# Optimization experiments

Measured on AMD Instinct MI355X. Metric: run time of the kernel, lower is better.

The kernel has to match this reference:

```python
import jax, jax.numpy as jnp
import numpy as np

NUM_HEADS = 4
HEAD_DIM = 64
RHO = 0.1  # threshold_rho


def setup_inputs() -> dict:
    key = jax.random.key(0)
    k0, k1, k2, k3, k4 = jax.random.split(key, 5)
    B, L, D = 2, 225, 256  # grid_size=15 -> L=225
    Hd = NUM_HEADS * HEAD_DIM
    w_scale = 1.0 / np.sqrt(D)
    return {
        "x": jax.random.normal(k0, (B, L, D), dtype=jnp.float32),
        "Wq": jax.random.normal(k1, (Hd, D), dtype=jnp.float32) * w_scale,
        "Wk": jax.random.normal(k2, (Hd, D), dtype=jnp.float32) * w_scale,
        "Wv": jax.random.normal(k3, (Hd, D), dtype=jnp.float32) * w_scale,
        "Wo": jax.random.normal(k4, (D, Hd), dtype=jnp.float32) * w_scale,
    }


def reference(x, Wq, Wk, Wv, Wo):
    B, L, D = x.shape
    H, d = NUM_HEADS, HEAD_DIM
    # Projections (torch Linear: y = x @ W.T), split heads -> [B,H,L,d]
    q = (x @ Wq.T).reshape(B, L, H, d).transpose(0, 2, 1, 3)
    k = (x @ Wk.T).reshape(B, L, H, d).transpose(0, 2, 1, 3)
    v = (x @ Wv.T).reshape(B, L, H, d).transpose(0, 2, 1, 3)

    # Raw attention scores S = Q K^T  [B,H,L,L]
    S = jnp.einsum('bhid,bhjd->bhij', q, k)

    # Adjacency build: for each key column j, U_j = s_j s_j^T / d, zero diag,
    # keep entries > rho; A = mean over j. Vectorized over j: [B,H,Li,Lk,Lj].
    eye = jnp.eye(L, dtype=S.dtype)
    U = S[:, :, :, None, :] * S[:, :, None, :, :] / d      # [B,H,i,k,j]
    U = U * (1.0 - eye)[None, None, :, :, None]            # zero (i==k) diag
    A = jnp.where(U > RHO, U, 0.0).sum(axis=-1) / L        # [B,H,L,L]

    # Normalize: A_hat = D^-1/2 (A + I) D^-1/2
    A_tilde = A + eye
    deg = jnp.clip(A_tilde.sum(axis=-1, keepdims=True), 1e-6, None)
    d_inv_sqrt = deg ** -0.5
    A_hat = d_inv_sqrt * A_tilde * jnp.swapaxes(d_inv_sqrt, -1, -2)

    # Jump: Phi(S) = A_hat S A_hat^T, then scale and softmax-attend
    S_jump = jnp.einsum('bhij,bhjk,bhlk->bhil', A_hat, S, A_hat) / np.sqrt(d)
    attn = jax.nn.softmax(S_jump, axis=-1)
    out = jnp.einsum('bhij,bhjd->bhid', attn, v)           # [B,H,L,d]
    out = out.transpose(0, 2, 1, 3).reshape(B, L, H * d)
    return out @ Wo.T
```

## Files before the change

### kernel.cpp

```cpp
#include <hip/hip_runtime.h>
#include <math.h>

#define B_  2
#define L_  225
#define D_  256
#define H_  4
#define DH_ 64
#define BH_ (B_*H_)
#define M_  (B_*L_)
#define LL_ (L_*L_)
#define RHO 0.1f
#define INV_D 0.015625f
#define INV_L (1.0f/225.0f)
#define INV_SQRT_D 0.125f

__global__ __launch_bounds__(256) void k_qkv(
    const float* __restrict__ x, const float* __restrict__ Wq,
    const float* __restrict__ Wk, const float* __restrict__ Wv,
    float* __restrict__ q, float* __restrict__ k, float* __restrict__ v)
{
    const int which = blockIdx.z;
    const float* W = (which == 0) ? Wq : (which == 1) ? Wk : Wv;
    float* out = (which == 0) ? q : (which == 1) ? k : v;
    const int m0 = blockIdx.x * 32;
    const int n0 = blockIdx.y * 32;
    __shared__ float Xs[32][33];
    __shared__ float Ws[32][33];
    const int t = threadIdx.x;
    const int ty = t >> 4, tx = t & 15;
    float acc[2][2] = {};
    for (int kt = 0; kt < D_; kt += 32) {
        #pragma unroll
        for (int i = 0; i < 4; ++i) {
            int li = t + i * 256;
            int r = li >> 5, c = li & 31;
            int m = m0 + r;
            Xs[r][c] = (m < M_) ? x[m * D_ + kt + c] : 0.f;
            Ws[r][c] = W[(n0 + r) * D_ + kt + c];
        }
        __syncthreads();
        #pragma unroll
        for (int kk = 0; kk < 32; ++kk) {
            float a0 = Xs[ty*2+0][kk], a1 = Xs[ty*2+1][kk];
            float b0 = Ws[tx*2+0][kk], b1 = Ws[tx*2+1][kk];
            acc[0][0] += a0*b0; acc[0][1] += a0*b1;
            acc[1][0] += a1*b0; acc[1][1] += a1*b1;
        }
        __syncthreads();
    }
    #pragma unroll
    for (int i = 0; i < 2; ++i) {
        int m = m0 + ty*2 + i;
        if (m >= M_) continue;
        int b = m / L_, l = m % L_;
        #pragma unroll
        for (int j = 0; j < 2; ++j) {
            int n = n0 + tx*2 + j;
            int h = n >> 6, dd = n & 63;
            out[((b * H_ + h) * L_ + l) * DH_ + dd] = acc[i][j];
        }
    }
}

__global__ __launch_bounds__(256) void k_scores(
    const float* __restrict__ q, const float* __restrict__ kk_,
    float* __restrict__ S)
{
    const int bh = blockIdx.z;
    const int i0 = blockIdx.x * 32, j0 = blockIdx.y * 32;
    __shared__ float Qs[32][65], Ks[32][65];
    const float* qb = q + bh * L_ * DH_;
    const float* kb = kk_ + bh * L_ * DH_;
    const int t = threadIdx.x;
    #pragma unroll
    for (int i = 0; i < 8; ++i) {
        int li = t + i * 256;
        int r = li >> 6, c = li & 63;
        Qs[r][c] = (i0 + r < L_) ? qb[(i0 + r) * DH_ + c] : 0.f;
        Ks[r][c] = (j0 + r < L_) ? kb[(j0 + r) * DH_ + c] : 0.f;
    }
    __syncthreads();
    const int ty = t >> 4, tx = t & 15;
    float acc[2][2] = {};
    #pragma unroll
    for (int c = 0; c < 64; ++c) {
        float a0 = Qs[ty*2+0][c], a1 = Qs[ty*2+1][c];
        float b0 = Ks[tx*2+0][c], b1 = Ks[tx*2+1][c];
        acc[0][0] += a0*b0; acc[0][1] += a0*b1;
        acc[1][0] += a1*b0; acc[1][1] += a1*b1;
    }
    float* Sb = S + bh * LL_;
    #pragma unroll
    for (int i = 0; i < 2; ++i) {
        int gi = i0 + ty*2 + i;
        if (gi >= L_) continue;
        #pragma unroll
        for (int j = 0; j < 2; ++j) {
            int gj = j0 + tx*2 + j;
            if (gj < L_) Sb[gi * L_ + gj] = acc[i][j];
        }
    }
}

__global__ __launch_bounds__(256) void k_adj(
    const float* __restrict__ S, float* __restrict__ A)
{
    const int bh = blockIdx.z;
    const int i0 = blockIdx.x * 32, k0 = blockIdx.y * 32;
    __shared__ float Si[32][65], Sk[32][65];
    const float* Sb = S + bh * LL_;
    const int t = threadIdx.x;
    const int ii = t & 31, kk0 = (t >> 5) * 4;
    float acc[4] = {};
    for (int jc = 0; jc < L_; jc += 64) {
        #pragma unroll
        for (int i = 0; i < 8; ++i) {
            int li = t + i * 256;
            int r = li >> 6, c = li & 63;
            int j = jc + c;
            Si[r][c] = (i0 + r < L_ && j < L_) ? Sb[(i0 + r) * L_ + j] : 0.f;
            Sk[r][c] = (k0 + r < L_ && j < L_) ? Sb[(k0 + r) * L_ + j] : 0.f;
        }
        __syncthreads();
        #pragma unroll 8
        for (int j = 0; j < 64; ++j) {
            float si = Si[ii][j];
            #pragma unroll
            for (int c = 0; c < 4; ++c) {
                float u = si * Sk[kk0 + c][j] * INV_D;
                acc[c] += (u > RHO) ? u : 0.f;
            }
        }
        __syncthreads();
    }
    int gi = i0 + ii;
    if (gi < L_) {
        float* Ab = A + bh * LL_ + gi * L_;
        #pragma unroll
        for (int c = 0; c < 4; ++c) {
            int gk = k0 + kk0 + c;
            if (gk < L_) Ab[gk] = (gi == gk) ? 0.f : acc[c] * INV_L;
        }
    }
}

__global__ __launch_bounds__(256) void k_dinv(
    const float* __restrict__ A, float* __restrict__ dinv)
{
    int bh = blockIdx.x;
    int i = threadIdx.x;
    if (i >= L_) return;
    const float* Ab = A + bh * LL_ + i * L_;
    float s = 1.0f;
    for (int kx = 0; kx < L_; ++kx) s += Ab[kx];
    s = fmaxf(s, 1e-6f);
    dinv[bh * L_ + i] = 1.0f / sqrtf(s);
}

__global__ __launch_bounds__(256) void k_ahat(
    const float* __restrict__ A, const float* __restrict__ dinv,
    float* __restrict__ Ahat)
{
    int e = blockIdx.x * 256 + threadIdx.x;
    if (e >= BH_ * LL_) return;
    int bh = e / LL_;
    int rem = e - bh * LL_;
    int r = rem / L_;
    int c = rem - r * L_;
    float val = A[e] + ((r == c) ? 1.f : 0.f);
    Ahat[e] = val * dinv[bh * L_ + r] * dinv[bh * L_ + c];
}

__global__ __launch_bounds__(256) void k_m1(
    const float* __restrict__ Ahat, const float* __restrict__ S,
    float* __restrict__ M1)
{
    const int bh = blockIdx.z;
    const int i0 = blockIdx.x * 32, c0 = blockIdx.y * 32;
    __shared__ float As[32][33], Bs[32][33];
    const float* Ab = Ahat + bh * LL_;
    const float* Sb = S + bh * LL_;
    const int t = threadIdx.x;
    const int ty = t >> 4, tx = t & 15;
    float acc[2][2] = {};
    for (int jt = 0; jt < L_; jt += 32) {
        #pragma unroll
        for (int i = 0; i < 4; ++i) {
            int li = t + i * 256;
            int r = li >> 5, c = li & 31;
            As[r][c] = (i0 + r < L_ && jt + c < L_) ? Ab[(i0 + r) * L_ + jt + c] : 0.f;
            Bs[r][c] = (jt + r < L_ && c0 + c < L_) ? Sb[(jt + r) * L_ + c0 + c] : 0.f;
        }
        __syncthreads();
        #pragma unroll
        for (int kk = 0; kk < 32; ++kk) {
            float a0 = As[ty*2+0][kk], a1 = As[ty*2+1][kk];
            float b0 = Bs[kk][tx*2+0], b1 = Bs[kk][tx*2+1];
            acc[0][0] += a0*b0; acc[0][1] += a0*b1;
            acc[1][0] += a1*b0; acc[1][1] += a1*b1;
        }
        __syncthreads();
    }
    float* Mb = M1 + bh * LL_;
    #pragma unroll
    for (int i = 0; i < 2; ++i) {
        int gi = i0 + ty*2 + i;
        if (gi >= L_) continue;
        #pragma unroll
        for (int j = 0; j < 2; ++j) {
            int gc = c0 + tx*2 + j;
            if (gc < L_) Mb[gi * L_ + gc] = acc[i][j];
        }
    }
}

__global__ __launch_bounds__(256) void k_sjump(
    const float* __restrict__ M1, const float* __restrict__ Ahat,
    float* __restrict__ attn)
{
    const int bh = blockIdx.z;
    const int i0 = blockIdx.x * 32, l0 = blockIdx.y * 32;
    __shared__ float As[32][33], Bs[32][33];
    const float* Mb = M1 + bh * LL_;
    const float* Ab = Ahat + bh * LL_;
    const int t = threadIdx.x;
    const int ty = t >> 4, tx = t & 15;
    float acc[2][2] = {};
    for (int jt = 0; jt < L_; jt += 32) {
        #pragma unroll
        for (int i = 0; i < 4; ++i) {
            int li = t + i * 256;
            int r = li >> 5, c = li & 31;
            As[r][c] = (i0 + r < L_ && jt + c < L_) ? Mb[(i0 + r) * L_ + jt + c] : 0.f;
            Bs[r][c] = (l0 + r < L_ && jt + c < L_) ? Ab[(l0 + r) * L_ + jt + c] : 0.f;
        }
        __syncthreads();
        #pragma unroll
        for (int kk = 0; kk < 32; ++kk) {
            float a0 = As[ty*2+0][kk], a1 = As[ty*2+1][kk];
            float b0 = Bs[tx*2+0][kk], b1 = Bs[tx*2+1][kk];
            acc[0][0] += a0*b0; acc[0][1] += a0*b1;
            acc[1][0] += a1*b0; acc[1][1] += a1*b1;
        }
        __syncthreads();
    }
    float* ob = attn + bh * LL_;
    #pragma unroll
    for (int i = 0; i < 2; ++i) {
        int gi = i0 + ty*2 + i;
        if (gi >= L_) continue;
        #pragma unroll
        for (int j = 0; j < 2; ++j) {
            int gl = l0 + tx*2 + j;
            if (gl < L_) ob[gi * L_ + gl] = acc[i][j] * INV_SQRT_D;
        }
    }
}

__global__ __launch_bounds__(256) void k_softmax(float* __restrict__ attn)
{
    const int bh = blockIdx.y, i = blockIdx.x;
    float* row = attn + bh * LL_ + i * L_;
    const int t = threadIdx.x;
    __shared__ float red[256];
    float v = (t < L_) ? row[t] : -INFINITY;
    red[t] = v;
    __syncthreads();
    for (int s = 128; s > 0; s >>= 1) {
        if (t < s) red[t] = fmaxf(red[t], red[t + s]);
        __syncthreads();
    }
    float m = red[0];
    __syncthreads();
    float e = (t < L_) ? expf(v - m) : 0.f;
    red[t] = e;
    __syncthreads();
    for (int s = 128; s > 0; s >>= 1) {
        if (t < s) red[t] += red[t + s];
        __syncthreads();
    }
    float inv = 1.0f / red[0];
    if (t < L_) row[t] = e * inv;
}

__global__ __launch_bounds__(256) void k_av(
    const float* __restrict__ attn, const float* __restrict__ v,
    float* __restrict__ oh)
{
    const int bh = blockIdx.y, i0 = blockIdx.x * 32;
    __shared__ float As[32][33];
    __shared__ float Vs[32][64];
    const float* ab = attn + bh * LL_;
    const float* vb = v + bh * L_ * DH_;
    const int t = threadIdx.x;
    const int dd = t & 63, iy0 = (t >> 6) * 8;
    float acc[8] = {};
    for (int lc = 0; lc < L_; lc += 32) {
        #pragma unroll
        for (int x2 = 0; x2 < 4; ++x2) {
            int li = t + x2 * 256;
            int r = li >> 5, c = li & 31;
            As[r][c] = (i0 + r < L_ && lc + c < L_) ? ab[(i0 + r) * L_ + lc + c] : 0.f;
        }
        #pragma unroll
        for (int x2 = 0; x2 < 8; ++x2) {
            int li = t + x2 * 256;
            int r = li >> 6, c = li & 63;
            Vs[r][c] = (lc + r < L_) ? vb[(lc + r) * DH_ + c] : 0.f;
        }
        __syncthreads();
        #pragma unroll
        for (int ll = 0; ll < 32; ++ll) {
            float vv = Vs[ll][dd];
            #pragma unroll
            for (int r = 0; r < 8; ++r) acc[r] += As[iy0 + r][ll] * vv;
        }
        __syncthreads();
    }
    const int b = bh >> 2, h = bh & 3;
    #pragma unroll
    for (int r = 0; r < 8; ++r) {
        int i = i0 + iy0 + r;
        if (i < L_) oh[(b * L_ + i) * (H_ * DH_) + h * DH_ + dd] = acc[r];
    }
}

__global__ __launch_bounds__(256) void k_out(
    const float* __restrict__ oh, const float* __restrict__ Wo,
    float* __restrict__ out)
{
    const int m0 = blockIdx.x * 32;
    const int n0 = blockIdx.y * 32;
    __shared__ float Xs[32][33];
    __shared__ float Ws[32][33];
    const int t = threadIdx.x;
    const int ty = t >> 4, tx = t & 15;
    float acc[2][2] = {};
    for (int kt = 0; kt < D_; kt += 32) {
        #pragma unroll
        for (int i = 0; i < 4; ++i) {
            int li = t + i * 256;
            int r = li >> 5, c = li & 31;
            int m = m0 + r;
            Xs[r][c] = (m < M_) ? oh[m * D_ + kt + c] : 0.f;
            Ws[r][c] = Wo[(n0 + r) * D_ + kt + c];
        }
        __syncthreads();
        #pragma unroll
        for (int kk = 0; kk < 32; ++kk) {
            float a0 = Xs[ty*2+0][kk], a1 = Xs[ty*2+1][kk];
            float b0 = Ws[tx*2+0][kk], b1 = Ws[tx*2+1][kk];
            acc[0][0] += a0*b0; acc[0][1] += a0*b1;
            acc[1][0] += a1*b0; acc[1][1] += a1*b1;
        }
        __syncthreads();
    }
    #pragma unroll
    for (int i = 0; i < 2; ++i) {
        int m = m0 + ty*2 + i;
        if (m >= M_) continue;
        #pragma unroll
        for (int j = 0; j < 2; ++j) {
            int n = n0 + tx*2 + j;
            out[m * D_ + n] = acc[i][j];
        }
    }
}

extern "C" void kernel_launch(void* const* d_in, const int* in_sizes, int n_in,
                              void* d_out, int out_size, void* d_ws, size_t ws_size,
                              hipStream_t stream)
{
    const float* x  = (const float*)d_in[0];
    const float* Wq = (const float*)d_in[1];
    const float* Wk = (const float*)d_in[2];
    const float* Wv = (const float*)d_in[3];
    const float* Wo = (const float*)d_in[4];
    float* out = (float*)d_out;

    float* ws   = (float*)d_ws;
    float* q    = ws;
    float* k    = q    + B_*H_*L_*DH_;
    float* v    = k    + B_*H_*L_*DH_;
    float* S    = v    + B_*H_*L_*DH_;
    float* A    = S    + BH_*LL_;
    float* Ahat = A    + BH_*LL_;
    float* M1   = Ahat + BH_*LL_;
    float* attn = M1   + BH_*LL_;
    float* dinv = attn + BH_*LL_;
    float* oh   = dinv + BH_*L_;

    dim3 blk(256);
    dim3 g1((M_ + 31) / 32, D_ / 32, 3);
    k_qkv<<<g1, blk, 0, stream>>>(x, Wq, Wk, Wv, q, k, v);

    dim3 g2(8, 8, BH_);
    k_scores<<<g2, blk, 0, stream>>>(q, k, S);

    dim3 g3(8, 8, BH_);
    k_adj<<<g3, blk, 0, stream>>>(S, A);

    k_dinv<<<dim3(BH_), blk, 0, stream>>>(A, dinv);

    k_ahat<<<dim3((BH_ * LL_ + 255) / 256), blk, 0, stream>>>(A, dinv, Ahat);

    dim3 g5(8, 8, BH_);
    k_m1<<<g5, blk, 0, stream>>>(Ahat, S, M1);

    dim3 g6(8, 8, BH_);
    k_sjump<<<g6, blk, 0, stream>>>(M1, Ahat, attn);

    dim3 g6b(L_, BH_);
    k_softmax<<<g6b, blk, 0, stream>>>(attn);

    dim3 g7(8, BH_);
    k_av<<<g7, blk, 0, stream>>>(attn, v, oh);

    dim3 g8((M_ + 31) / 32, D_ / 32);
    k_out<<<g8, blk, 0, stream>>>(oh, Wo, out);
}
```

Baseline: 248.0 us.

## Fuse degree normalization into adjacency and GEMMs, fuse softmax with AV, vectorize loads

Result: faster. 199.0 us (-19.8%).

```diff
diff --git a/kernel.cpp b/kernel.cpp
--- a/kernel.cpp
+++ b/kernel.cpp
@@ -10,34 +10,41 @@
 #define M_  (B_*L_)
 #define LL_ (L_*L_)
 #define RHO 0.1f
-#define INV_D 0.015625f
 #define INV_L (1.0f/225.0f)
 #define INV_SQRT_D 0.125f
+
+__device__ __forceinline__ float dinv_of(const float* deg, int idx) {
+    return 1.0f / sqrtf(fmaxf(deg[idx], 1e-6f));
+}
 
 __global__ __launch_bounds__(256) void k_qkv(
     const float* __restrict__ x, const float* __restrict__ Wq,
     const float* __restrict__ Wk, const float* __restrict__ Wv,
-    float* __restrict__ q, float* __restrict__ k, float* __restrict__ v)
-{
+    float* __restrict__ q, float* __restrict__ k, float* __restrict__ v,
+    float* __restrict__ deg)
+{
+    const int t = threadIdx.x;
+    if (blockIdx.z == 0 && blockIdx.y == 0 && t < 128) {
+        int idx = blockIdx.x * 128 + t;
+        if (idx < BH_ * L_) deg[idx] = 1.0f;
+    }
     const int which = blockIdx.z;
     const float* W = (which == 0) ? Wq : (which == 1) ? Wk : Wv;
     float* out = (which == 0) ? q : (which == 1) ? k : v;
     const int m0 = blockIdx.x * 32;
     const int n0 = blockIdx.y * 32;
-    __shared__ float Xs[32][33];
-    __shared__ float Ws[32][33];
-    const int t = threadIdx.x;
-    const int ty = t >> 4, tx = t & 15;
+    __shared__ float Xs[32][36];
+    __shared__ float Ws[32][36];
+    const int ty = t >> 4, tx = t & 15;
+    const int sr = t >> 3, sc4 = (t & 7) * 4;
     float acc[2][2] = {};
     for (int kt = 0; kt < D_; kt += 32) {
-        #pragma unroll
-        for (int i = 0; i < 4; ++i) {
-            int li = t + i * 256;
-            int r = li >> 5, c = li & 31;
-            int m = m0 + r;
-            Xs[r][c] = (m < M_) ? x[m * D_ + kt + c] : 0.f;
-            Ws[r][c] = W[(n0 + r) * D_ + kt + c];
-        }
+        int m = m0 + sr;
+        float4 xv = (m < M_) ? *(const float4*)&x[m * D_ + kt + sc4]
+                             : make_float4(0.f, 0.f, 0.f, 0.f);
+        float4 wv = *(const float4*)&W[(n0 + sr) * D_ + kt + sc4];
+        *(float4*)&Xs[sr][sc4] = xv;
+        *(float4*)&Ws[sr][sc4] = wv;
         __syncthreads();
         #pragma unroll
         for (int kk = 0; kk < 32; ++kk) {
@@ -68,16 +75,20 @@
 {
     const int bh = blockIdx.z;
     const int i0 = blockIdx.x * 32, j0 = blockIdx.y * 32;
-    __shared__ float Qs[32][65], Ks[32][65];
+    __shared__ float Qs[32][68], Ks[32][68];
     const float* qb = q + bh * L_ * DH_;
     const float* kb = kk_ + bh * L_ * DH_;
     const int t = threadIdx.x;
     #pragma unroll
-    for (int i = 0; i < 8; ++i) {
-        int li = t + i * 256;
-        int r = li >> 6, c = li & 63;
-        Qs[r][c] = (i0 + r < L_) ? qb[(i0 + r) * DH_ + c] : 0.f;
-        Ks[r][c] = (j0 + r < L_) ? kb[(j0 + r) * DH_ + c] : 0.f;
+    for (int s = 0; s < 2; ++s) {
+        int li = t + s * 256;
+        int r = li >> 4, c4 = (li & 15) * 4;
+        float4 qv = (i0 + r < L_) ? *(const float4*)&qb[(i0 + r) * DH_ + c4]
+                                  : make_float4(0.f,0.f,0.f,0.f);
+        float4 kv = (j0 + r < L_) ? *(const float4*)&kb[(j0 + r) * DH_ + c4]
+                                  : make_float4(0.f,0.f,0.f,0.f);
+        *(float4*)&Qs[r][c4] = qv;
+        *(float4*)&Ks[r][c4] = kv;
     }
     __syncthreads();
     const int ty = t >> 4, tx = t & 15;
@@ -103,101 +114,98 @@
 }
 
 __global__ __launch_bounds__(256) void k_adj(
-    const float* __restrict__ S, float* __restrict__ A)
+    const float* __restrict__ S, float* __restrict__ A, float* __restrict__ deg)
 {
     const int bh = blockIdx.z;
     const int i0 = blockIdx.x * 32, k0 = blockIdx.y * 32;
-    __shared__ float Si[32][65], Sk[32][65];
+    __shared__ float SiT[32][34], SkT[32][34];
     const float* Sb = S + bh * LL_;
     const int t = threadIdx.x;
-    const int ii = t & 31, kk0 = (t >> 5) * 4;
-    float acc[4] = {};
-    for (int jc = 0; jc < L_; jc += 64) {
-        #pragma unroll
-        for (int i = 0; i < 8; ++i) {
-            int li = t + i * 256;
-            int r = li >> 6, c = li & 63;
+    const int tx = t & 15, ty = t >> 4;
+    float a00 = 0.f, a01 = 0.f, a10 = 0.f, a11 = 0.f;
+    for (int jc = 0; jc < L_; jc += 32) {
+        #pragma unroll
+        for (int s = 0; s < 4; ++s) {
+            int li = t + s * 256;
+            int r = li >> 5, c = li & 31;
             int j = jc + c;
-            Si[r][c] = (i0 + r < L_ && j < L_) ? Sb[(i0 + r) * L_ + j] : 0.f;
-            Sk[r][c] = (k0 + r < L_ && j < L_) ? Sb[(k0 + r) * L_ + j] : 0.f;
-        }
-        __syncthreads();
-        #pragma unroll 8
-        for (int j = 0; j < 64; ++j) {
-            float si = Si[ii][j];
-            #pragma unroll
-            for (int c = 0; c < 4; ++c) {
-                float u = si * Sk[kk0 + c][j] * INV_D;
-                acc[c] += (u > RHO) ? u : 0.f;
-            }
-        }
-        __syncthreads();
-    }
-    int gi = i0 + ii;
-    if (gi < L_) {
-        float* Ab = A + bh * LL_ + gi * L_;
-        #pragma unroll
-        for (int c = 0; c < 4; ++c) {
-            int gk = k0 + kk0 + c;
-            if (gk < L_) Ab[gk] = (gi == gk) ? 0.f : acc[c] * INV_L;
-        }
-    }
-}
-
-__global__ __launch_bounds__(256) void k_dinv(
-    const float* __restrict__ A, float* __restrict__ dinv)
-{
-    int bh = blockIdx.x;
-    int i = threadIdx.x;
-    if (i >= L_) return;
-    const float* Ab = A + bh * LL_ + i * L_;
-    float s = 1.0f;
-    for (int kx = 0; kx < L_; ++kx) s += Ab[kx];
-    s = fmaxf(s, 1e-6f);
-    dinv[bh * L_ + i] = 1.0f / sqrtf(s);
-}
-
-__global__ __launch_bounds__(256) void k_ahat(
-    const float* __restrict__ A, const float* __restrict__ dinv,
-    float* __restrict__ Ahat)
-{
-    int e = blockIdx.x * 256 + threadIdx.x;
-    if (e >= BH_ * LL_) return;
-    int bh = e / LL_;
-    int rem = e - bh * LL_;
-    int r = rem / L_;
-    int c = rem - r * L_;
-    float val = A[e] + ((r == c) ? 1.f : 0.f);
-    Ahat[e] = val * dinv[bh * L_ + r] * dinv[bh * L_ + c];
+            SiT[c][r] = (i0 + r < L_ && j < L_) ? Sb[(i0 + r) * L_ + j] * 0.125f : 0.f;
+            SkT[c][r] = (k0 + r < L_ && j < L_) ? Sb[(k0 + r) * L_ + j] * 0.125f : 0.f;
+        }
+        __syncthreads();
+        #pragma unroll
+        for (int j = 0; j < 32; ++j) {
+            float2 a = *(const float2*)&SiT[j][ty * 2];
+            float2 b = *(const float2*)&SkT[j][tx * 2];
+            float u;
+            u = a.x * b.x; a00 += (u > RHO) ? u : 0.f;
+            u = a.x * b.y; a01 += (u > RHO) ? u : 0.f;
+            u = a.y * b.x; a10 += (u > RHO) ? u : 0.f;
+            u = a.y * b.y; a11 += (u > RHO) ? u : 0.f;
+        }
+        __syncthreads();
+    }
+    const int gi0 = i0 + ty * 2, gk0 = k0 + tx * 2;
+    float v00 = (gi0     < L_ && gk0     < L_ && gi0     != gk0    ) ? a00 * INV_L : 0.f;
+    float v01 = (gi0     < L_ && gk0 + 1 < L_ && gi0     != gk0 + 1) ? a01 * INV_L : 0.f;
+    float v10 = (gi0 + 1 < L_ && gk0     < L_ && gi0 + 1 != gk0    ) ? a10 * INV_L : 0.f;
+    float v11 = (gi0 + 1 < L_ && gk0 + 1 < L_ && gi0 + 1 != gk0 + 1) ? a11 * INV_L : 0.f;
+    float* Ab = A + bh * LL_;
+    if (gi0 < L_) {
+        if (gk0     < L_) Ab[gi0 * L_ + gk0    ] = v00;
+        if (gk0 + 1 < L_) Ab[gi0 * L_ + gk0 + 1] = v01;
+    }
+    if (gi0 + 1 < L_) {
+        if (gk0     < L_) Ab[(gi0+1) * L_ + gk0    ] = v10;
+        if (gk0 + 1 < L_) Ab[(gi0+1) * L_ + gk0 + 1] = v11;
+    }
+    float rs0 = v00 + v01, rs1 = v10 + v11;
+    #pragma unroll
+    for (int m = 1; m < 16; m <<= 1) {
+        rs0 += __shfl_xor(rs0, m);
+        rs1 += __shfl_xor(rs1, m);
+    }
+    if (tx == 0) {
+        if (gi0     < L_) atomicAdd(&deg[bh * L_ + gi0    ], rs0);
+        if (gi0 + 1 < L_) atomicAdd(&deg[bh * L_ + gi0 + 1], rs1);
+    }
 }
 
 __global__ __launch_bounds__(256) void k_m1(
-    const float* __restrict__ Ahat, const float* __restrict__ S,
-    float* __restrict__ M1)
+    const float* __restrict__ A, const float* __restrict__ S,
+    const float* __restrict__ deg, float* __restrict__ M1)
 {
     const int bh = blockIdx.z;
     const int i0 = blockIdx.x * 32, c0 = blockIdx.y * 32;
-    __shared__ float As[32][33], Bs[32][33];
-    const float* Ab = Ahat + bh * LL_;
+    __shared__ float As[32][33];
+    __shared__ float Ss[32][34];
+    const float* Ab = A + bh * LL_;
     const float* Sb = S + bh * LL_;
+    const float* db = deg + bh * L_;
     const int t = threadIdx.x;
     const int ty = t >> 4, tx = t & 15;
     float acc[2][2] = {};
     for (int jt = 0; jt < L_; jt += 32) {
         #pragma unroll
-        for (int i = 0; i < 4; ++i) {
-            int li = t + i * 256;
+        for (int s = 0; s < 4; ++s) {
+            int li = t + s * 256;
             int r = li >> 5, c = li & 31;
-            As[r][c] = (i0 + r < L_ && jt + c < L_) ? Ab[(i0 + r) * L_ + jt + c] : 0.f;
-            Bs[r][c] = (jt + r < L_ && c0 + c < L_) ? Sb[(jt + r) * L_ + c0 + c] : 0.f;
+            int gi = i0 + r, gj = jt + c;
+            float av = (gi < L_ && gj < L_) ? Ab[gi * L_ + gj] : 0.f;
+            if (gi == gj && gi < L_) av += 1.f;
+            As[r][c] = av;
+            int gj2 = jt + r, gc = c0 + c;
+            float sv = 0.f;
+            if (gj2 < L_ && gc < L_) sv = Sb[gj2 * L_ + gc] * dinv_of(db, gj2);
+            Ss[r][c] = sv;
         }
         __syncthreads();
         #pragma unroll
         for (int kk = 0; kk < 32; ++kk) {
             float a0 = As[ty*2+0][kk], a1 = As[ty*2+1][kk];
-            float b0 = Bs[kk][tx*2+0], b1 = Bs[kk][tx*2+1];
-            acc[0][0] += a0*b0; acc[0][1] += a0*b1;
-            acc[1][0] += a1*b0; acc[1][1] += a1*b1;
+            float2 b = *(const float2*)&Ss[kk][tx * 2];
+            acc[0][0] += a0*b.x; acc[0][1] += a0*b.y;
+            acc[1][0] += a1*b.x; acc[1][1] += a1*b.y;
         }
         __syncthreads();
     }
@@ -206,38 +214,49 @@
     for (int i = 0; i < 2; ++i) {
         int gi = i0 + ty*2 + i;
         if (gi >= L_) continue;
+        float dvi = dinv_of(db, gi);
         #pragma unroll
         for (int j = 0; j < 2; ++j) {
             int gc = c0 + tx*2 + j;
-            if (gc < L_) Mb[gi * L_ + gc] = acc[i][j];
+            if (gc < L_) Mb[gi * L_ + gc] = acc[i][j] * dvi;
         }
     }
 }
 
 __global__ __launch_bounds__(256) void k_sjump(
-    const float* __restrict__ M1, const float* __restrict__ Ahat,
-    float* __restrict__ attn)
+    const float* __restrict__ M1, const float* __restrict__ A,
+    const float* __restrict__ deg, float* __restrict__ attn)
 {
     const int bh = blockIdx.z;
     const int i0 = blockIdx.x * 32, l0 = blockIdx.y * 32;
-    __shared__ float As[32][33], Bs[32][33];
+    __shared__ float Ms[32][33];
+    __shared__ float Bs[32][33];
     const float* Mb = M1 + bh * LL_;
-    const float* Ab = Ahat + bh * LL_;
+    const float* Ab = A + bh * LL_;
+    const float* db = deg + bh * L_;
     const int t = threadIdx.x;
     const int ty = t >> 4, tx = t & 15;
     float acc[2][2] = {};
     for (int jt = 0; jt < L_; jt += 32) {
         #pragma unroll
-        for (int i = 0; i < 4; ++i) {
-            int li = t + i * 256;
+        for (int s = 0; s < 4; ++s) {
+            int li = t + s * 256;
             int r = li >> 5, c = li & 31;
-            As[r][c] = (i0 + r < L_ && jt + c < L_) ? Mb[(i0 + r) * L_ + jt + c] : 0.f;
-            Bs[r][c] = (l0 + r < L_ && jt + c < L_) ? Ab[(l0 + r) * L_ + jt + c] : 0.f;
+            int gi = i0 + r, gj = jt + c;
+            Ms[r][c] = (gi < L_ && gj < L_) ? Mb[gi * L_ + gj] : 0.f;
+            int gl = l0 + r;
+            float bv = 0.f;
+            if (gl < L_ && gj < L_) {
+                bv = Ab[gl * L_ + gj];
+                if (gl == gj) bv += 1.f;
+                bv *= dinv_of(db, gj);
+            }
+            Bs[r][c] = bv;
         }
         __syncthreads();
         #pragma unroll
         for (int kk = 0; kk < 32; ++kk) {
-            float a0 = As[ty*2+0][kk], a1 = As[ty*2+1][kk];
+            float a0 = Ms[ty*2+0][kk], a1 = Ms[ty*2+1][kk];
             float b0 = Bs[tx*2+0][kk], b1 = Bs[tx*2+1][kk];
             acc[0][0] += a0*b0; acc[0][1] += a0*b1;
             acc[1][0] += a1*b0; acc[1][1] += a1*b1;
@@ -252,76 +271,57 @@
         #pragma unroll
         for (int j = 0; j < 2; ++j) {
             int gl = l0 + tx*2 + j;
-            if (gl < L_) ob[gi * L_ + gl] = acc[i][j] * INV_SQRT_D;
-        }
-    }
-}
-
-__global__ __launch_bounds__(256) void k_softmax(float* __restrict__ attn)
-{
-    const int bh = blockIdx.y, i = blockIdx.x;
-    float* row = attn + bh * LL_ + i * L_;
-    const int t = threadIdx.x;
-    __shared__ float red[256];
-    float v = (t < L_) ? row[t] : -INFINITY;
-    red[t] = v;
+            if (gl < L_) ob[gi * L_ + gl] = acc[i][j] * dinv_of(db, gl) * INV_SQRT_D;
+        }
+    }
+}
+
+__global__ __launch_bounds__(256) void k_smav(
+    const float* __restrict__ sj, const float* __restrict__ v,
+    float* __restrict__ oh)
+{
+    const int bh = blockIdx.y, i0 = blockIdx.x * 16;
+    __shared__ float P[16][226];
+    __shared__ float rinv[16];
+    const float* sb = sj + bh * LL_;
+    const float* vb = v + bh * L_ * DH_;
+    const int t = threadIdx.x;
+    for (int e = t; e < 16 * L_; e += 256) {
+        int r = e / L_, c = e - r * L_;
+        int gi = i0 + r;
+        P[r][c] = (gi < L_) ? sb[gi * L_ + c] : 0.f;
+    }
     __syncthreads();
-    for (int s = 128; s > 0; s >>= 1) {
-        if (t < s) red[t] = fmaxf(red[t], red[t + s]);
-        __syncthreads();
-    }
-    float m = red[0];
+    {
+        const int r = t >> 4, lane = t & 15;
+        float m = -INFINITY;
+        for (int c = lane; c < L_; c += 16) m = fmaxf(m, P[r][c]);
+        #pragma unroll
+        for (int mk = 1; mk < 16; mk <<= 1) m = fmaxf(m, __shfl_xor(m, mk));
+        float ssum = 0.f;
+        for (int c = lane; c < L_; c += 16) {
+            float e = expf(P[r][c] - m);
+            P[r][c] = e;
+            ssum += e;
+        }
+        #pragma unroll
+        for (int mk = 1; mk < 16; mk <<= 1) ssum += __shfl_xor(ssum, mk);
+        if (lane == 0) rinv[r] = 1.0f / ssum;
+    }
     __syncthreads();
-    float e = (t < L_) ? expf(v - m) : 0.f;
-    red[t] = e;
-    __syncthreads();
-    for (int s = 128; s > 0; s >>= 1) {
-        if (t < s) red[t] += red[t + s];
-        __syncthreads();
-    }
-    float inv = 1.0f / red[0];
-    if (t < L_) row[t] = e * inv;
-}
-
-__global__ __launch_bounds__(256) void k_av(
-    const float* __restrict__ attn, const float* __restrict__ v,
-    float* __restrict__ oh)
-{
-    const int bh = blockIdx.y, i0 = blockIdx.x * 32;
-    __shared__ float As[32][33];
-    __shared__ float Vs[32][64];
-    const float* ab = attn + bh * LL_;
-    const float* vb = v + bh * L_ * DH_;
-    const int t = threadIdx.x;
-    const int dd = t & 63, iy0 = (t >> 6) * 8;
-    float acc[8] = {};
-    for (int lc = 0; lc < L_; lc += 32) {
-        #pragma unroll
-        for (int x2 = 0; x2 < 4; ++x2) {
-            int li = t + x2 * 256;
-            int r = li >> 5, c = li & 31;
-            As[r][c] = (i0 + r < L_ && lc + c < L_) ? ab[(i0 + r) * L_ + lc + c] : 0.f;
-        }
-        #pragma unroll
-        for (int x2 = 0; x2 < 8; ++x2) {
-            int li = t + x2 * 256;
-            int r = li >> 6, c = li & 63;
-            Vs[r][c] = (lc + r < L_) ? vb[(lc + r) * DH_ + c] : 0.f;
-        }
-        __syncthreads();
-        #pragma unroll
-        for (int ll = 0; ll < 32; ++ll) {
-            float vv = Vs[ll][dd];
-            #pragma unroll
-            for (int r = 0; r < 8; ++r) acc[r] += As[iy0 + r][ll] * vv;
-        }
-        __syncthreads();
+    const int dd = t & 63, rg = t >> 6;
+    float acc[4] = {};
+    for (int l = 0; l < L_; ++l) {
+        float vv = vb[l * DH_ + dd];
+        #pragma unroll
+        for (int u = 0; u < 4; ++u) acc[u] += P[rg * 4 + u][l] * vv;
     }
     const int b = bh >> 2, h = bh & 3;
     #pragma unroll
-    for (int r = 0; r < 8; ++r) {
-        int i = i0 + iy0 + r;
-        if (i < L_) oh[(b * L_ + i) * (H_ * DH_) + h * DH_ + dd] = acc[r];
+    for (int u = 0; u < 4; ++u) {
+        int r = rg * 4 + u;
+        int gi = i0 + r;
+        if (gi < L_) oh[(b * L_ + gi) * (H_ * DH_) + h * DH_ + dd] = acc[u] * rinv[r];
     }
 }
 
@@ -331,20 +331,19 @@
 {
     const int m0 = blockIdx.x * 32;
     const int n0 = blockIdx.y * 32;
-    __shared__ float Xs[32][33];
-    __shared__ float Ws[32][33];
-    const int t = threadIdx.x;
-    const int ty = t >> 4, tx = t & 15;
+    __shared__ float Xs[32][36];
+    __shared__ float Ws[32][36];
+    const int t = threadIdx.x;
+    const int ty = t >> 4, tx = t & 15;
+    const int sr = t >> 3, sc4 = (t & 7) * 4;
     float acc[2][2] = {};
     for (int kt = 0; kt < D_; kt += 32) {
-        #pragma unroll
-        for (int i = 0; i < 4; ++i) {
-            int li = t + i * 256;
-            int r = li >> 5, c = li & 31;
-            int m = m0 + r;
-            Xs[r][c] = (m < M_) ? oh[m * D_ + kt + c] : 0.f;
-            Ws[r][c] = Wo[(n0 + r) * D_ + kt + c];
-        }
+        int m = m0 + sr;
+        float4 xv = (m < M_) ? *(const float4*)&oh[m * D_ + kt + sc4]
+                             : make_float4(0.f,0.f,0.f,0.f);
+        float4 wv = *(const float4*)&Wo[(n0 + sr) * D_ + kt + sc4];
+        *(float4*)&Xs[sr][sc4] = xv;
+        *(float4*)&Ws[sr][sc4] = wv;
         __syncthreads();
         #pragma unroll
         for (int kk = 0; kk < 32; ++kk) {
@@ -384,38 +383,17 @@
     float* v    = k    + B_*H_*L_*DH_;
     float* S    = v    + B_*H_*L_*DH_;
     float* A    = S    + BH_*LL_;
-    float* Ahat = A    + BH_*LL_;
-    float* M1   = Ahat + BH_*LL_;
+    float* M1   = A    + BH_*LL_;
     float* attn = M1   + BH_*LL_;
-    float* dinv = attn + BH_*LL_;
-    float* oh   = dinv + BH_*L_;
+    float* deg  = attn + BH_*LL_;
+    float* oh   = deg  + BH_*L_;
 
     dim3 blk(256);
-    dim3 g1((M_ + 31) / 32, D_ / 32, 3);
-    k_qkv<<<g1, blk, 0, stream>>>(x, Wq, Wk, Wv, q, k, v);
-
-    dim3 g2(8, 8, BH_);
-    k_scores<<<g2, blk, 0, stream>>>(q, k, S);
-
-    dim3 g3(8, 8, BH_);
-    k_adj<<<g3, blk, 0, stream>>>(S, A);
-
-    k_dinv<<<dim3(BH_), blk, 0, stream>>>(A, dinv);
-
-    k_ahat<<<dim3((BH_ * LL_ + 255) / 256), blk, 0, stream>>>(A, dinv, Ahat);
-
-    dim3 g5(8, 8, BH_);
-    k_m1<<<g5, blk, 0, stream>>>(Ahat, S, M1);
-
-    dim3 g6(8, 8, BH_);
-    k_sjump<<<g6, blk, 0, stream>>>(M1, Ahat, attn);
-
-    dim3 g6b(L_, BH_);
-    k_softmax<<<g6b, blk, 0, stream>>>(attn);
-
-    dim3 g7(8, BH_);
-    k_av<<<g7, blk, 0, stream>>>(attn, v, oh);
-
-    dim3 g8((M_ + 31) / 32, D_ / 32);
-    k_out<<<g8, blk, 0, stream>>>(oh, Wo, out);
-}
+    k_qkv   <<<dim3(15, 8, 3), blk, 0, stream>>>(x, Wq, Wk, Wv, q, k, v, deg);
+    k_scores<<<dim3(8, 8, BH_), blk, 0, stream>>>(q, k, S);
+    k_adj   <<<dim3(8, 8, BH_), blk, 0, stream>>>(S, A, deg);
+    k_m1    <<<dim3(8, 8, BH_), blk, 0, stream>>>(A, S, deg, M1);
+    k_sjump <<<dim3(8, 8, BH_), blk, 0, stream>>>(M1, A, deg, attn);
+    k_smav  <<<dim3(15, BH_), blk, 0, stream>>>(attn, v, oh);
+    k_out   <<<dim3(15, 8), blk, 0, stream>>>(oh, Wo, out);
+}
```
